# Performance work log

Measured on AMD Instinct MI355X. Metric: run time of the kernel, lower is better.

The kernel has to match this reference:

```python
import jax, jax.numpy as jnp
import numpy as np

D_MODEL = 1024
NHEAD = 16
D_HEAD = D_MODEL // NHEAD


def setup_inputs() -> dict:
    key = jax.random.key(0)
    ks = jax.random.split(key, 9)
    B, S = 2, 2048
    scale = 1.0 / np.sqrt(D_MODEL)
    x = jax.random.normal(ks[0], (B, S, D_MODEL), dtype=jnp.float32)
    Wq = jax.random.normal(ks[1], (D_MODEL, D_MODEL), dtype=jnp.float32) * scale
    Wk = jax.random.normal(ks[2], (D_MODEL, D_MODEL), dtype=jnp.float32) * scale
    Wv = jax.random.normal(ks[3], (D_MODEL, D_MODEL), dtype=jnp.float32) * scale
    Wo = jax.random.normal(ks[4], (D_MODEL, D_MODEL), dtype=jnp.float32) * scale
    bq = jax.random.normal(ks[5], (D_MODEL,), dtype=jnp.float32) * 0.01
    bk = jax.random.normal(ks[6], (D_MODEL,), dtype=jnp.float32) * 0.01
    bv = jax.random.normal(ks[7], (D_MODEL,), dtype=jnp.float32) * 0.01
    bo = jax.random.normal(ks[8], (D_MODEL,), dtype=jnp.float32) * 0.01
    return {"x": x, "Wq": Wq, "bq": bq, "Wk": Wk, "bk": bk,
            "Wv": Wv, "bv": bv, "Wo": Wo, "bo": bo}


def reference(x, Wq, bq, Wk, bk, Wv, bv, Wo, bo):
    B, S, D = x.shape
    H, Dh = NHEAD, D_HEAD
    # projections; weights stored as (in, out) so y = x @ W + b
    def split_heads(t):  # [B,S,D] -> [B,H,S,Dh]
        return t.reshape(B, S, H, Dh).transpose(0, 2, 1, 3)
    q = split_heads(x @ Wq + bq)
    k = split_heads(x @ Wk + bk)
    v = split_heads(x @ Wv + bv)
    scale = 1.0 / jnp.sqrt(jnp.asarray(Dh, dtype=x.dtype))
    attn = jnp.einsum("bhqd,bhkd->bhqk", q, k) * scale  # [B,H,S,S]
    attn = jax.nn.softmax(attn, axis=-1)
    out = jnp.einsum("bhqk,bhkd->bhqd", attn, v)  # [B,H,S,Dh]
    out = out.transpose(0, 2, 1, 3).reshape(B, S, D)
    return out @ Wo + bo
```

## Files before the change

kernel.cpp:

```cpp
#include <hip/hip_runtime.h>
#include <hip/hip_bf16.h>
#include <stdint.h>
#include <stddef.h>

typedef __bf16 b16;
typedef __bf16 b16x4 __attribute__((ext_vector_type(4)));
typedef __bf16 b16x8 __attribute__((ext_vector_type(8)));
typedef float  f32x4 __attribute__((ext_vector_type(4)));

#define LOG2E 1.4426950408889634f
#define QSCALE (0.125f * LOG2E)

#if __has_builtin(__builtin_amdgcn_exp2f)
#define EXP2F(x) __builtin_amdgcn_exp2f(x)
#else
#define EXP2F(x) exp2f(x)
#endif

typedef __attribute__((address_space(1))) void gvoid;
typedef __attribute__((address_space(3))) void svoid;

__device__ __forceinline__ void async_cp16(void* lds, const void* g) {
    __builtin_amdgcn_global_load_lds((gvoid*)(void*)g, (svoid*)lds, 16, 0, 0);
}

#define SW(r) ((((r) & 7)) ^ (((r) >> 1) & 4))

__global__ __launch_bounds__(256) void k_prep(const float* __restrict__ x,
                                              const float* __restrict__ Wq,
                                              const float* __restrict__ Wk,
                                              const float* __restrict__ Wv,
                                              const float* __restrict__ Wo,
                                              b16* __restrict__ Xb,
                                              b16* __restrict__ WtQKV,
                                              b16* __restrict__ Wot) {
    const int z = blockIdx.z;
    if (z == 4) {
        const int blk = blockIdx.y * 32 + blockIdx.x;
        const float* src = x + (size_t)blk * 4096;
        b16* dst = Xb + (size_t)blk * 4096;
#pragma unroll
        for (int c = 0; c < 4; ++c) {
            const int i = c * 1024 + threadIdx.x * 4;
            float4 v = *(const float4*)(src + i);
            b16x4 o = { (b16)v.x, (b16)v.y, (b16)v.z, (b16)v.w };
            *(b16x4*)(dst + i) = o;
        }
        return;
    }
    __shared__ float t[32][33];
    const float* W = (z == 0) ? Wq : (z == 1) ? Wk : (z == 2) ? Wv : Wo;
    const int k0 = blockIdx.x * 32, n0 = blockIdx.y * 32;
    const int tr = threadIdx.x >> 3, tc4 = (threadIdx.x & 7) * 4;
    float4 v = *(const float4*)(W + (size_t)(k0 + tr) * 1024 + n0 + tc4);
    t[tr][tc4 + 0] = v.x; t[tr][tc4 + 1] = v.y;
    t[tr][tc4 + 2] = v.z; t[tr][tc4 + 3] = v.w;
    __syncthreads();
    b16* dst = (z < 3) ? (WtQKV + ((size_t)z << 20)) : Wot;
    b16x4 o = { (b16)t[tc4 + 0][tr], (b16)t[tc4 + 1][tr],
                (b16)t[tc4 + 2][tr], (b16)t[tc4 + 3][tr] };
    *(b16x4*)(dst + (size_t)(n0 + tr) * 1024 + k0 + tc4) = o;
}

__device__ __forceinline__ void gemm128_core(const b16* __restrict__ Ag,
                                             const b16* __restrict__ Bg,
                                             b16* As, b16* Bs, int tid,
                                             f32x4 acc[4][4]) {
    const int lane = tid & 63, wave = tid >> 6;
    const int wm = wave & 1, wn = wave >> 1;
    const int quad = lane >> 4, lc = lane & 15;
    const int ci0 = tid, ci1 = tid + 256;
    const b16* a0 = Ag + (ci0 >> 2) * 1024 + (ci0 & 3) * 8;
    const b16* a1 = Ag + (ci1 >> 2) * 1024 + (ci1 & 3) * 8;
    const b16* b0 = Bg + (ci0 >> 2) * 1024 + (ci0 & 3) * 8;
    const b16* b1 = Bg + (ci1 >> 2) * 1024 + (ci1 & 3) * 8;

#define GSTAGE(BUF, K0) do {                                   \
        async_cp16(As + (BUF) * 4096 + ci0 * 8, a0 + (K0));    \
        async_cp16(As + (BUF) * 4096 + ci1 * 8, a1 + (K0));    \
        async_cp16(Bs + (BUF) * 4096 + ci0 * 8, b0 + (K0));    \
        async_cp16(Bs + (BUF) * 4096 + ci1 * 8, b1 + (K0));    \
    } while (0)

#define GSTEP(BUF, SBUF, SK0, VM, DOSTAGE) do {                          \
        if (DOSTAGE) GSTAGE(SBUF, SK0);                                  \
        asm volatile("s_waitcnt vmcnt(" #VM ")" ::: "memory");           \
        __builtin_amdgcn_s_barrier();                                    \
        __builtin_amdgcn_sched_barrier(0);                               \
        b16x8 af[4], bfr[4];                                             \
        const b16* Al = As + (BUF) * 4096;                               \
        const b16* Bl = Bs + (BUF) * 4096;                               \
        _Pragma("unroll")                                                \
        for (int mt = 0; mt < 4; ++mt)                                   \
            af[mt] = *(const b16x8*)(Al + (wm * 64 + mt * 16 + lc) * 32 + quad * 8); \
        _Pragma("unroll")                                                \
        for (int nt = 0; nt < 4; ++nt)                                   \
            bfr[nt] = *(const b16x8*)(Bl + (wn * 64 + nt * 16 + lc) * 32 + quad * 8); \
        asm volatile("s_waitcnt lgkmcnt(0)" ::: "memory");               \
        __builtin_amdgcn_sched_barrier(0);                               \
        __builtin_amdgcn_s_barrier();                                    \
        __builtin_amdgcn_s_setprio(1);                                   \
        _Pragma("unroll")                                                \
        for (int mt = 0; mt < 4; ++mt)                                   \
            _Pragma("unroll")                                            \
            for (int nt = 0; nt < 4; ++nt)                               \
                acc[mt][nt] = __builtin_amdgcn_mfma_f32_16x16x32_bf16(   \
                    af[mt], bfr[nt], acc[mt][nt], 0, 0, 0);              \
        __builtin_amdgcn_s_setprio(0);                                   \
    } while (0)

    GSTAGE(0, 0);
    GSTAGE(1, 32);
    for (int i = 0; i < 10; ++i) {
        const int kb = 96 * i;
        GSTEP(0, 2, kb + 64, 8, 1);
        GSTEP(1, 0, kb + 96, 8, 1);
        GSTEP(2, 1, kb + 128, 8, 1);
    }
    GSTEP(0, 0, 0, 4, 0);
    GSTEP(1, 0, 0, 0, 0);
#undef GSTEP
#undef GSTAGE
}

__global__ __launch_bounds__(256, 3) void k_gemm_qkv(
    const b16* __restrict__ A, const b16* __restrict__ Bt,
    const float* __restrict__ bq, const float* __restrict__ bk,
    const float* __restrict__ bv,
    b16* __restrict__ Qg, b16* __restrict__ Kg, b16* __restrict__ Vtg) {
    __shared__ __align__(16) b16 LB[24576];
    b16* As = LB;
    b16* Bs = LB + 12288;
    char* Tb = (char*)LB;
    const int bm = blockIdx.x, bn = blockIdx.y;
    const int tid = threadIdx.x;
    const int lane = tid & 63, wave = tid >> 6;
    const int wm = wave & 1, wn = wave >> 1;
    const int quad = lane >> 4, lc = lane & 15;

    f32x4 acc[4][4] = {};
    gemm128_core(A + (size_t)(bm * 128) * 1024, Bt + (size_t)(bn * 128) * 1024,
                 As, Bs, tid, acc);

    const int mat = bn >> 3;
    const float* bp = (mat == 0) ? bq : (mat == 1) ? bk : bv;
    const float scl = (mat == 0) ? QSCALE : 1.0f;

#pragma unroll
    for (int nt = 0; nt < 4; ++nt) {
        const int ln = wn * 64 + nt * 16 + lc;
        const float bval = bp[(bn * 128 + ln) & 1023];
#pragma unroll
        for (int mt = 0; mt < 4; ++mt) {
            const int lm = wm * 64 + mt * 16 + quad * 4;
            if (mat == 2) {
                b16x4 o;
#pragma unroll
                for (int r = 0; r < 4; ++r) o[r] = (b16)(acc[mt][nt][r] + bval);
                const int byte = ln * 256 + (((lm >> 3) ^ (ln & 15)) << 4) + (lm & 7) * 2;
                *(b16x4*)(Tb + byte) = o;
            } else {
#pragma unroll
                for (int r = 0; r < 4; ++r) {
                    const int row = lm + r;
                    const int byte = row * 256 + (((ln >> 3) ^ (row & 15)) << 4) + (ln & 7) * 2;
                    *(b16*)(Tb + byte) = (b16)((acc[mt][nt][r] + bval) * scl);
                }
            }
        }
    }
    __syncthreads();

    const int chunk = tid & 7, hr0 = tid >> 3;
    const int b = bm >> 4;
    const int s_blk = (bm * 128) & 2047;
#pragma unroll
    for (int p = 0; p < 8; ++p) {
        const int hr = p * 32 + hr0;
        const int row = hr >> 1, half = hr & 1;
        const int c2 = (half * 8 + chunk) ^ (row & 15);
        b16x8 v = *(const b16x8*)(Tb + row * 256 + c2 * 16);
        if (mat == 2) {
            const int cm = (bn * 128 + row) & 1023;
            const int h = cm >> 6, dh = cm & 63;
            *(b16x8*)(Vtg + (size_t)((b * 16 + h) * 64 + dh) * 2048 +
                      s_blk + half * 64 + chunk * 8) = v;
        } else {
            const int s = s_blk + row;
            const int cm = (bn * 128 + half * 64 + chunk * 8) & 1023;
            const int h = cm >> 6, dh = cm & 63;
            b16* dst = (mat == 0) ? Qg : Kg;
            *(b16x8*)(dst + ((size_t)(b * 16 + h) * 2048 + s) * 64 + dh) = v;
        }
    }
}

__global__ __launch_bounds__(256, 4) void k_flash(
    const b16* __restrict__ Qg, const b16* __restrict__ Kg,
    const b16* __restrict__ Vtg, b16* __restrict__ AO) {
    __shared__ __align__(16) b16 Ks[2 * 64 * 64];
    __shared__ __align__(16) b16 Vs[2 * 64 * 64];
    __shared__ float Lred[4][16];

    const int bid = blockIdx.x;
    const int qb = bid >> 5;
    const int bh = bid & 31;

    const int tid = threadIdx.x, lane = tid & 63, wave = tid >> 6;
    const int quad = lane >> 4, lc = lane & 15;

    const b16* Kbh = Kg + (size_t)bh * 2048 * 64;
    const b16* Vbh = Vtg + (size_t)bh * 64 * 2048;

    const int ci0 = tid, ci1 = tid + 256;
    const int r0 = ci0 >> 3, gc0 = (ci0 & 7) ^ SW(r0);
    const int r1 = ci1 >> 3, gc1 = (ci1 & 7) ^ SW(r1);
    const b16* pK0 = Kbh + r0 * 64 + gc0 * 8;
    const b16* pK1 = Kbh + r1 * 64 + gc1 * 8;
    const b16* pV0 = Vbh + (size_t)r0 * 2048 + gc0 * 8;
    const b16* pV1 = Vbh + (size_t)r1 * 2048 + gc1 * 8;

#define FSTAGE(BUF) do {                                   \
        async_cp16(Ks + (BUF) * 4096 + ci0 * 8, pK0);      \
        async_cp16(Ks + (BUF) * 4096 + ci1 * 8, pK1);      \
        async_cp16(Vs + (BUF) * 4096 + ci0 * 8, pV0);      \
        async_cp16(Vs + (BUF) * 4096 + ci1 * 8, pV1);      \
        pK0 += 4096; pK1 += 4096; pV0 += 64; pV1 += 64;    \
    } while (0)

    FSTAGE(0);

    const b16* Qbase = Qg + ((size_t)bh * 2048 + qb * 64 + wave * 16) * 64;
    b16x8 qf0 = *(const b16x8*)(Qbase + lc * 64 + quad * 8);
    b16x8 qf1 = *(const b16x8*)(Qbase + lc * 64 + 32 + quad * 8);

    f32x4 oacc[4] = {};
    float lsum = 0.f;

    auto flash_tile = [&](const b16* Kc, const b16* Vc) {
#pragma unroll
        for (int ks = 0; ks < 2; ++ks) {
            b16x8 pf;
#pragma unroll
            for (int t = 0; t < 2; ++t) {
                const int krow = ks * 32 + (lc >> 2) * 8 + t * 4 + (lc & 3);
                b16x8 kf0 = *(const b16x8*)(Kc + krow * 64 + ((0 * 4 + quad) ^ SW(krow)) * 8);
                b16x8 kf1 = *(const b16x8*)(Kc + krow * 64 + ((1 * 4 + quad) ^ SW(krow)) * 8);
                f32x4 s = {};
                __builtin_amdgcn_s_setprio(1);
                s = __builtin_amdgcn_mfma_f32_16x16x32_bf16(kf0, qf0, s, 0, 0, 0);
                s = __builtin_amdgcn_mfma_f32_16x16x32_bf16(kf1, qf1, s, 0, 0, 0);
                __builtin_amdgcn_s_setprio(0);
                float e0 = EXP2F(s[0]), e1 = EXP2F(s[1]);
                float e2 = EXP2F(s[2]), e3 = EXP2F(s[3]);
                lsum += (e0 + e1) + (e2 + e3);
                pf[t * 4 + 0] = (b16)e0;
                pf[t * 4 + 1] = (b16)e1;
                pf[t * 4 + 2] = (b16)e2;
                pf[t * 4 + 3] = (b16)e3;
            }
            b16x8 vf[4];
#pragma unroll
            for (int dt = 0; dt < 4; ++dt) {
                const int row = dt * 16 + lc;
                vf[dt] = *(const b16x8*)(Vc + row * 64 + ((ks * 4 + quad) ^ SW(row)) * 8);
            }
            __builtin_amdgcn_s_setprio(1);
#pragma unroll
            for (int dt = 0; dt < 4; ++dt)
                oacc[dt] = __builtin_amdgcn_mfma_f32_16x16x32_bf16(
                    pf, vf[dt], oacc[dt], 0, 0, 0);
            __builtin_amdgcn_s_setprio(0);
        }
    };

    for (int kt = 0; kt < 32; kt += 2) {
        FSTAGE(1);
        asm volatile("s_waitcnt vmcnt(4)" ::: "memory");
        __builtin_amdgcn_s_barrier();
        __builtin_amdgcn_sched_barrier(0);
        flash_tile(Ks, Vs);
        __builtin_amdgcn_sched_barrier(0);
        __builtin_amdgcn_s_barrier();
        if (kt + 2 < 32) {
            FSTAGE(0);
            asm volatile("s_waitcnt vmcnt(4)" ::: "memory");
        } else {
            asm volatile("s_waitcnt vmcnt(0)" ::: "memory");
        }
        __builtin_amdgcn_s_barrier();
        __builtin_amdgcn_sched_barrier(0);
        flash_tile(Ks + 4096, Vs + 4096);
        __builtin_amdgcn_sched_barrier(0);
        __builtin_amdgcn_s_barrier();
    }
#undef FSTAGE

    lsum += __shfl_xor(lsum, 16, 64);
    lsum += __shfl_xor(lsum, 32, 64);

    if (quad == 0) Lred[wave][lc] = lsum;
    const int b = bh >> 4, h = bh & 15;
#pragma unroll
    for (int r = 0; r < 4; ++r) {
        const float inv = 1.0f / Lred[wave][quad * 4 + r];
        const int s = qb * 64 + wave * 16 + quad * 4 + r;
#pragma unroll
        for (int dt = 0; dt < 4; ++dt)
            AO[(size_t)(b * 2048 + s) * 1024 + h * 64 + dt * 16 + lc] =
                (b16)(oacc[dt][r] * inv);
    }
}

__global__ __launch_bounds__(256, 3) void k_gemm_out(
    const b16* __restrict__ A, const b16* __restrict__ Bt,
    const float* __restrict__ bo, float* __restrict__ out) {
    __shared__ __align__(16) b16 As[3 * 128 * 32];
    __shared__ __align__(16) b16 Bs[3 * 128 * 32];
    const int bm = blockIdx.x, bn = blockIdx.y;
    const int tid = threadIdx.x;
    const int lane = tid & 63, wave = tid >> 6;
    const int wm = wave & 1, wn = wave >> 1;
    const int quad = lane >> 4, lc = lane & 15;

    f32x4 acc[4][4] = {};
    gemm128_core(A + (size_t)(bm * 128) * 1024, Bt + (size_t)(bn * 128) * 1024,
                 As, Bs, tid, acc);

#pragma unroll
    for (int nt = 0; nt < 4; ++nt) {
        const int n = bn * 128 + wn * 64 + nt * 16 + lc;
        const float bval = bo[n];
#pragma unroll
        for (int mt = 0; mt < 4; ++mt) {
            const int m0 = bm * 128 + wm * 64 + mt * 16 + quad * 4;
#pragma unroll
            for (int r = 0; r < 4; ++r)
                out[(size_t)(m0 + r) * 1024 + n] = acc[mt][nt][r] + bval;
        }
    }
}

extern "C" void kernel_launch(void* const* d_in, const int* in_sizes, int n_in,
                              void* d_out, int out_size, void* d_ws, size_t ws_size,
                              hipStream_t stream) {
    const float* x  = (const float*)d_in[0];
    const float* Wq = (const float*)d_in[1];
    const float* bq = (const float*)d_in[2];
    const float* Wk = (const float*)d_in[3];
    const float* bk = (const float*)d_in[4];
    const float* Wv = (const float*)d_in[5];
    const float* bv = (const float*)d_in[6];
    const float* Wo = (const float*)d_in[7];
    const float* bo = (const float*)d_in[8];
    float* out = (float*)d_out;

    char* ws = (char*)d_ws;
    const size_t MB = 1024 * 1024;
    b16* Xb  = (b16*)(ws);
    b16* AO  = (b16*)(ws);
    b16* WtQ = (b16*)(ws + 8 * MB);
    b16* Wot = (b16*)(ws + 14 * MB);
    b16* Qg  = (b16*)(ws + 16 * MB);
    b16* Kg  = (b16*)(ws + 24 * MB);
    b16* Vtg = (b16*)(ws + 32 * MB);

    k_prep<<<dim3(32, 32, 5), 256, 0, stream>>>(x, Wq, Wk, Wv, Wo, Xb, WtQ, Wot);
    k_gemm_qkv<<<dim3(32, 24), 256, 0, stream>>>(Xb, WtQ, bq, bk, bv, Qg, Kg, Vtg);
    k_flash<<<dim3(1024), 256, 0, stream>>>(Qg, Kg, Vtg, AO);
    k_gemm_out<<<dim3(32, 8), 256, 0, stream>>>(AO, Wot, bo, out);
}
```

Baseline: 189.6 us.

## Widen flash attention query tile per wave to reuse K/V fragments

Each wave in the attention kernel now handles 64 query rows (four 16-row subtiles) instead of 16, and a block holds 2 waves covering 128 queries, so the grid is halved to 512 blocks of 128 threads. Every K and V fragment read from LDS now feeds four MFMA chains instead of one, which cuts LDS traffic and global K/V staging per query. The cost is much higher register pressure from the 4x4 accumulator array and the extra Q fragments, which may reduce occupancy. Fewer blocks also means less parallelism across CUs.

```diff
diff --git a/kernel.cpp b/kernel.cpp
--- a/kernel.cpp
+++ b/kernel.cpp
@@ -195,12 +195,12 @@
     }
 }
 
-__global__ __launch_bounds__(256, 4) void k_flash(
+__global__ __launch_bounds__(128, 2) void k_flash(
     const b16* __restrict__ Qg, const b16* __restrict__ Kg,
     const b16* __restrict__ Vtg, b16* __restrict__ AO) {
     __shared__ __align__(16) b16 Ks[2 * 64 * 64];
     __shared__ __align__(16) b16 Vs[2 * 64 * 64];
-    __shared__ float Lred[4][16];
+    __shared__ float Lred[2][64];
 
     const int bid = blockIdx.x;
     const int qb = bid >> 5;
@@ -212,52 +212,62 @@
     const b16* Kbh = Kg + (size_t)bh * 2048 * 64;
     const b16* Vbh = Vtg + (size_t)bh * 64 * 2048;
 
-    const int ci0 = tid, ci1 = tid + 256;
-    const int r0 = ci0 >> 3, gc0 = (ci0 & 7) ^ SW(r0);
-    const int r1 = ci1 >> 3, gc1 = (ci1 & 7) ^ SW(r1);
-    const b16* pK0 = Kbh + r0 * 64 + gc0 * 8;
-    const b16* pK1 = Kbh + r1 * 64 + gc1 * 8;
-    const b16* pV0 = Vbh + (size_t)r0 * 2048 + gc0 * 8;
-    const b16* pV1 = Vbh + (size_t)r1 * 2048 + gc1 * 8;
-
-#define FSTAGE(BUF) do {                                   \
-        async_cp16(Ks + (BUF) * 4096 + ci0 * 8, pK0);      \
-        async_cp16(Ks + (BUF) * 4096 + ci1 * 8, pK1);      \
-        async_cp16(Vs + (BUF) * 4096 + ci0 * 8, pV0);      \
-        async_cp16(Vs + (BUF) * 4096 + ci1 * 8, pV1);      \
-        pK0 += 4096; pK1 += 4096; pV0 += 64; pV1 += 64;    \
+    const b16* pK[4];
+    const b16* pV[4];
+    int ci[4];
+#pragma unroll
+    for (int j = 0; j < 4; ++j) {
+        ci[j] = tid + j * 128;
+        const int r = ci[j] >> 3, cs = ci[j] & 7;
+        const int gc = cs ^ SW(r);
+        pK[j] = Kbh + r * 64 + gc * 8;
+        pV[j] = Vbh + (size_t)r * 2048 + gc * 8;
+    }
+
+#define FSTAGE(BUF) do {                                       \
+        _Pragma("unroll")                                      \
+        for (int j = 0; j < 4; ++j) {                          \
+            async_cp16(Ks + (BUF) * 4096 + ci[j] * 8, pK[j]);  \
+            async_cp16(Vs + (BUF) * 4096 + ci[j] * 8, pV[j]);  \
+            pK[j] += 4096; pV[j] += 64;                        \
+        }                                                      \
     } while (0)
 
     FSTAGE(0);
 
-    const b16* Qbase = Qg + ((size_t)bh * 2048 + qb * 64 + wave * 16) * 64;
-    b16x8 qf0 = *(const b16x8*)(Qbase + lc * 64 + quad * 8);
-    b16x8 qf1 = *(const b16x8*)(Qbase + lc * 64 + 32 + quad * 8);
-
-    f32x4 oacc[4] = {};
-    float lsum = 0.f;
+    const b16* Qbase = Qg + ((size_t)bh * 2048 + qb * 128 + wave * 64) * 64;
+    b16x8 qf[4][2];
+#pragma unroll
+    for (int qt = 0; qt < 4; ++qt)
+#pragma unroll
+        for (int ch = 0; ch < 2; ++ch)
+            qf[qt][ch] = *(const b16x8*)(Qbase + (qt * 16 + lc) * 64 + ch * 32 + quad * 8);
+
+    f32x4 oacc[4][4] = {};
+    float lsum[4] = {0.f, 0.f, 0.f, 0.f};
 
     auto flash_tile = [&](const b16* Kc, const b16* Vc) {
 #pragma unroll
         for (int ks = 0; ks < 2; ++ks) {
-            b16x8 pf;
+            b16x8 pf[4];
 #pragma unroll
             for (int t = 0; t < 2; ++t) {
                 const int krow = ks * 32 + (lc >> 2) * 8 + t * 4 + (lc & 3);
                 b16x8 kf0 = *(const b16x8*)(Kc + krow * 64 + ((0 * 4 + quad) ^ SW(krow)) * 8);
                 b16x8 kf1 = *(const b16x8*)(Kc + krow * 64 + ((1 * 4 + quad) ^ SW(krow)) * 8);
-                f32x4 s = {};
-                __builtin_amdgcn_s_setprio(1);
-                s = __builtin_amdgcn_mfma_f32_16x16x32_bf16(kf0, qf0, s, 0, 0, 0);
-                s = __builtin_amdgcn_mfma_f32_16x16x32_bf16(kf1, qf1, s, 0, 0, 0);
-                __builtin_amdgcn_s_setprio(0);
-                float e0 = EXP2F(s[0]), e1 = EXP2F(s[1]);
-                float e2 = EXP2F(s[2]), e3 = EXP2F(s[3]);
-                lsum += (e0 + e1) + (e2 + e3);
-                pf[t * 4 + 0] = (b16)e0;
-                pf[t * 4 + 1] = (b16)e1;
-                pf[t * 4 + 2] = (b16)e2;
-                pf[t * 4 + 3] = (b16)e3;
+#pragma unroll
+                for (int qt = 0; qt < 4; ++qt) {
+                    f32x4 s = {};
+                    s = __builtin_amdgcn_mfma_f32_16x16x32_bf16(kf0, qf[qt][0], s, 0, 0, 0);
+                    s = __builtin_amdgcn_mfma_f32_16x16x32_bf16(kf1, qf[qt][1], s, 0, 0, 0);
+                    float e0 = EXP2F(s[0]), e1 = EXP2F(s[1]);
+                    float e2 = EXP2F(s[2]), e3 = EXP2F(s[3]);
+                    lsum[qt] += (e0 + e1) + (e2 + e3);
+                    pf[qt][t * 4 + 0] = (b16)e0;
+                    pf[qt][t * 4 + 1] = (b16)e1;
+                    pf[qt][t * 4 + 2] = (b16)e2;
+                    pf[qt][t * 4 + 3] = (b16)e3;
+                }
             }
             b16x8 vf[4];
 #pragma unroll
@@ -267,16 +277,18 @@
             }
             __builtin_amdgcn_s_setprio(1);
 #pragma unroll
-            for (int dt = 0; dt < 4; ++dt)
-                oacc[dt] = __builtin_amdgcn_mfma_f32_16x16x32_bf16(
-                    pf, vf[dt], oacc[dt], 0, 0, 0);
+            for (int qt = 0; qt < 4; ++qt)
+#pragma unroll
+                for (int dt = 0; dt < 4; ++dt)
+                    oacc[qt][dt] = __builtin_amdgcn_mfma_f32_16x16x32_bf16(
+                        pf[qt], vf[dt], oacc[qt][dt], 0, 0, 0);
             __builtin_amdgcn_s_setprio(0);
         }
     };
 
     for (int kt = 0; kt < 32; kt += 2) {
         FSTAGE(1);
-        asm volatile("s_waitcnt vmcnt(4)" ::: "memory");
+        asm volatile("s_waitcnt vmcnt(8)" ::: "memory");
         __builtin_amdgcn_s_barrier();
         __builtin_amdgcn_sched_barrier(0);
         flash_tile(Ks, Vs);
@@ -284,7 +296,7 @@
         __builtin_amdgcn_s_barrier();
         if (kt + 2 < 32) {
             FSTAGE(0);
-            asm volatile("s_waitcnt vmcnt(4)" ::: "memory");
+            asm volatile("s_waitcnt vmcnt(8)" ::: "memory");
         } else {
             asm volatile("s_waitcnt vmcnt(0)" ::: "memory");
         }
@@ -296,20 +308,28 @@
     }
 #undef FSTAGE
 
-    lsum += __shfl_xor(lsum, 16, 64);
-    lsum += __shfl_xor(lsum, 32, 64);
-
-    if (quad == 0) Lred[wave][lc] = lsum;
+#pragma unroll
+    for (int qt = 0; qt < 4; ++qt) {
+        lsum[qt] += __shfl_xor(lsum[qt], 16, 64);
+        lsum[qt] += __shfl_xor(lsum[qt], 32, 64);
+    }
+
+    if (quad == 0) {
+#pragma unroll
+        for (int qt = 0; qt < 4; ++qt) Lred[wave][qt * 16 + lc] = lsum[qt];
+    }
     const int b = bh >> 4, h = bh & 15;
 #pragma unroll
-    for (int r = 0; r < 4; ++r) {
-        const float inv = 1.0f / Lred[wave][quad * 4 + r];
-        const int s = qb * 64 + wave * 16 + quad * 4 + r;
-#pragma unroll
-        for (int dt = 0; dt < 4; ++dt)
-            AO[(size_t)(b * 2048 + s) * 1024 + h * 64 + dt * 16 + lc] =
-                (b16)(oacc[dt][r] * inv);
-    }
+    for (int qt = 0; qt < 4; ++qt)
+#pragma unroll
+        for (int r = 0; r < 4; ++r) {
+            const float inv = 1.0f / Lred[wave][qt * 16 + quad * 4 + r];
+            const int s = qb * 128 + wave * 64 + qt * 16 + quad * 4 + r;
+#pragma unroll
+            for (int dt = 0; dt < 4; ++dt)
+                AO[(size_t)(b * 2048 + s) * 1024 + h * 64 + dt * 16 + lc] =
+                    (b16)(oacc[qt][dt][r] * inv);
+        }
 }
 
 __global__ __launch_bounds__(256, 3) void k_gemm_out(
@@ -367,6 +387,6 @@
 
     k_prep<<<dim3(32, 32, 5), 256, 0, stream>>>(x, Wq, Wk, Wv, Wo, Xb, WtQ, Wot);
     k_gemm_qkv<<<dim3(32, 24), 256, 0, stream>>>(Xb, WtQ, bq, bk, bv, Qg, Kg, Vtg);
-    k_flash<<<dim3(1024), 256, 0, stream>>>(Qg, Kg, Vtg, AO);
+    k_flash<<<dim3(512), 128, 0, stream>>>(Qg, Kg, Vtg, AO);
     k_gemm_out<<<dim3(32, 8), 256, 0, stream>>>(AO, Wot, bo, out);
 }
```

Result: slower. 206.6 us (+8.9%).
